# Optimization experiments

Hardware: AMD Instinct MI355X
Metric: run time of the kernel (lower is better)

The kernel has to match this reference:

```python
import jax, jax.numpy as jnp
import numpy as np

VOCAB, E, H, OUT = 32000, 128, 128, 16
N, L = 8192, 32


def setup_inputs() -> dict:
    key = jax.random.key(0)
    ks = jax.random.split(key, 12)
    s_lstm = 1.0 / np.sqrt(H)
    s_g1 = 1.0 / np.sqrt(2 * H)
    s_g2 = 1.0 / np.sqrt(OUT)
    return {
        "tokens": jax.random.randint(ks[0], (N, L), 0, VOCAB, dtype=jnp.int64)
        if jax.config.read("jax_enable_x64") else jax.random.randint(ks[0], (N, L), 0, VOCAB, dtype=jnp.int32),
        "adj": jax.random.uniform(ks[1], (N, N), dtype=jnp.float32) / N,
        "embed_W": jax.random.normal(ks[2], (VOCAB, E), dtype=jnp.float32),
        "W_ih": jax.random.uniform(ks[3], (4 * H, E), jnp.float32, -s_lstm, s_lstm),
        "W_hh": jax.random.uniform(ks[4], (4 * H, H), jnp.float32, -s_lstm, s_lstm),
        "b_ih": jax.random.uniform(ks[5], (4 * H,), jnp.float32, -s_lstm, s_lstm),
        "b_hh": jax.random.uniform(ks[6], (4 * H,), jnp.float32, -s_lstm, s_lstm),
        "gc1_W": jax.random.uniform(ks[7], (H, 2 * H), jnp.float32, -s_g1, s_g1),
        "gc1_b": jax.random.uniform(ks[8], (2 * H,), jnp.float32, -s_g1, s_g1),
        "gc2_W": jax.random.uniform(ks[9], (2 * H, OUT), jnp.float32, -s_g2, s_g2),
        "gc2_b": jax.random.uniform(ks[10], (OUT,), jnp.float32, -s_g2, s_g2),
    }


def _lstm_final_h(x, W_ih, W_hh, b_ih, b_hh):
    # x: [N, L, E] -> final hidden state [N, H] (torch gate order i,f,g,o)
    Hd = W_hh.shape[1]
    # precompute input projections for all timesteps: [L, N, 4H]
    xi = jnp.einsum('nle,ge->lng', x, W_ih) + b_ih + b_hh

    def step(carry, xt):
        h, c = carry
        gates = xt + h @ W_hh.T
        i, f, g, o = jnp.split(gates, 4, axis=-1)
        i, f, o = jax.nn.sigmoid(i), jax.nn.sigmoid(f), jax.nn.sigmoid(o)
        g = jnp.tanh(g)
        c = f * c + i * g
        h = o * jnp.tanh(c)
        return (h, c), None

    n = x.shape[0]
    h0 = jnp.zeros((n, Hd), x.dtype)
    (h, _), _ = jax.lax.scan(step, (h0, h0), xi)
    return h


def reference(tokens, adj, embed_W, W_ih, W_hh, b_ih, b_hh, gc1_W, gc1_b, gc2_W, gc2_b):
    x = embed_W[tokens]                                  # [N, L, E]
    feat = _lstm_final_h(x, W_ih, W_hh, b_ih, b_hh)      # [N, H]
    h1 = jax.nn.relu(adj @ (feat @ gc1_W) + gc1_b)       # [N, 2H]
    logits = adj @ (h1 @ gc2_W) + gc2_b                  # [N, OUT]
    return jax.nn.log_softmax(logits, axis=1)
```

## Files before the change

kernel.cpp:

```cpp
#include <hip/hip_runtime.h>

typedef __attribute__((ext_vector_type(8))) short bf16x8;
typedef __attribute__((ext_vector_type(4))) float f32x4;

__device__ __forceinline__ short f2bf(float f){
  union { float f; unsigned u; } v; v.f = f;
  unsigned r = v.u + 0x7fffu + ((v.u >> 16) & 1u);
  return (short)(r >> 16);
}
__device__ __forceinline__ bf16x8 pack8(float4 a, float4 b){
  bf16x8 v;
  v[0]=f2bf(a.x); v[1]=f2bf(a.y); v[2]=f2bf(a.z); v[3]=f2bf(a.w);
  v[4]=f2bf(b.x); v[5]=f2bf(b.y); v[6]=f2bf(b.z); v[7]=f2bf(b.w);
  return v;
}
__device__ __forceinline__ f32x4 mfma16(bf16x8 a, bf16x8 b, f32x4 c){
  return __builtin_amdgcn_mfma_f32_16x16x32_bf16(a, b, c, 0, 0, 0);
}
__device__ __forceinline__ float sigm(float x){
  return __builtin_amdgcn_rcpf(1.f + __expf(-x));
}
__device__ __forceinline__ float tanh_(float x){
  return 1.f - 2.f*__builtin_amdgcn_rcpf(1.f + __expf(2.f*x));
}

__global__ __launch_bounds__(512,2) void lstm_kernel(
    const int* __restrict__ tokens, const float* __restrict__ embed,
    const float* __restrict__ Wih, const float* __restrict__ Whh,
    const float* __restrict__ bih, const float* __restrict__ bhh,
    float* __restrict__ feat)
{
  __shared__ short hbuf[2*32*128];
  __shared__ short xbuf[2*32*128];
  __shared__ int   tokbuf[32*32];
  const int tid  = threadIdx.x;
  const int wave = tid >> 6, lane = tid & 63;
  const int l15  = lane & 15, lhi = lane >> 4;
  const int nbase = blockIdx.x * 32;
  const int ucol  = wave*16 + l15;

  bf16x8 wihf[4][4], whhf[4][4];
  #pragma unroll
  for(int g=0; g<4; ++g){
    const float* wi = Wih + (size_t)(g*128 + ucol)*128;
    const float* wh = Whh + (size_t)(g*128 + ucol)*128;
    #pragma unroll
    for(int kt=0; kt<4; ++kt){
      int e0 = kt*32 + lhi*8;
      float4 a0 = *(const float4*)(wi+e0), a1 = *(const float4*)(wi+e0+4);
      float4 b0 = *(const float4*)(wh+e0), b1 = *(const float4*)(wh+e0+4);
      wihf[g][kt] = pack8(a0,a1);
      whhf[g][kt] = pack8(b0,b1);
    }
  }
  float bs[4];
  #pragma unroll
  for(int g=0; g<4; ++g) bs[g] = bih[g*128+ucol] + bhh[g*128+ucol];

  for(int i=tid; i<1024; i+=512) tokbuf[i] = tokens[(size_t)nbase*32 + i];

  float c[2][4], hreg[2][4];
  #pragma unroll
  for(int m=0;m<2;++m) for(int r=0;r<4;++r){ c[m][r]=0.f; hreg[m][r]=0.f; }

  *(bf16x8*)((char*)hbuf + tid*16) = (bf16x8){0,0,0,0,0,0,0,0};
  __syncthreads();

  const int srow = tid >> 4, sseg = tid & 15;
  {
    int tok = tokbuf[srow*32 + 0];
    const float* e = embed + (size_t)tok*128 + sseg*8;
    float4 a = *(const float4*)e, b = *(const float4*)(e+4);
    int byte = (srow*256 + sseg*16) ^ ((srow&7)<<4);
    *(bf16x8*)((char*)xbuf + byte) = pack8(a,b);
  }
  __syncthreads();

  float4 sa, sb;
  #pragma unroll 1
  for(int l=0; l<32; ++l){
    if(l < 31){
      int tok = tokbuf[srow*32 + l + 1];
      const float* e = embed + (size_t)tok*128 + sseg*8;
      sa = *(const float4*)e; sb = *(const float4*)(e+4);
    }
    const char* hb = (const char*)hbuf + (l&1)*8192;
    const char* xb = (const char*)xbuf + (l&1)*8192;
    f32x4 acc[2][4];
    #pragma unroll
    for(int m=0;m<2;++m) for(int g=0;g<4;++g) acc[m][g]=(f32x4){0.f,0.f,0.f,0.f};
    #pragma unroll
    for(int kt=0; kt<4; ++kt){
      int cbyte = kt*64 + lhi*16;
      int swz = (l15&7)<<4;
      int a0 = (l15*256 + cbyte) ^ swz;
      int a1 = ((16+l15)*256 + cbyte) ^ swz;
      bf16x8 h0 = *(const bf16x8*)(hb + a0);
      bf16x8 h1 = *(const bf16x8*)(hb + a1);
      bf16x8 x0 = *(const bf16x8*)(xb + a0);
      bf16x8 x1 = *(const bf16x8*)(xb + a1);
      #pragma unroll
      for(int g=0; g<4; ++g){
        acc[0][g]=mfma16(h0, whhf[g][kt], acc[0][g]);
        acc[1][g]=mfma16(h1, whhf[g][kt], acc[1][g]);
        acc[0][g]=mfma16(x0, wihf[g][kt], acc[0][g]);
        acc[1][g]=mfma16(x1, wihf[g][kt], acc[1][g]);
      }
    }
    char* hn = (char*)hbuf + ((l+1)&1)*8192;
    #pragma unroll
    for(int m=0;m<2;++m){
      #pragma unroll
      for(int r=0;r<4;++r){
        float gi = acc[m][0][r] + bs[0];
        float gf = acc[m][1][r] + bs[1];
        float gg = acc[m][2][r] + bs[2];
        float go = acc[m][3][r] + bs[3];
        float i_ = sigm(gi), f_ = sigm(gf), o_ = sigm(go), g_ = tanh_(gg);
        float cc = f_*c[m][r] + i_*g_;
        c[m][r] = cc;
        float hh = o_*tanh_(cc);
        hreg[m][r] = hh;
        int row = m*16 + lhi*4 + r;
        int wb = (row*256 + ucol*2) ^ ((row&7)<<4);
        *(short*)(hn + wb) = f2bf(hh);
      }
    }
    if(l < 31){
      int byte = ((l+1)&1)*8192 + ((srow*256 + sseg*16) ^ ((srow&7)<<4));
      *(bf16x8*)((char*)xbuf + byte) = pack8(sa,sb);
    }
    __syncthreads();
  }
  #pragma unroll
  for(int m=0;m<2;++m) for(int r=0;r<4;++r){
    int row = nbase + m*16 + lhi*4 + r;
    feat[(size_t)row*128 + ucol] = hreg[m][r];
  }
}

__global__ __launch_bounds__(256) void gc1_kernel(
  const float* __restrict__ feat, const float* __restrict__ W1,
  short* __restrict__ Y1t)
{
  __shared__ float fs[128][36];
  int tid = threadIdx.x; int nb = blockIdx.x*32;
  #pragma unroll
  for(int i=0;i<4;++i){
    int idx = i*256 + tid;
    float4 v = ((const float4*)(feat + (size_t)nb*128))[idx];
    int n = idx>>5, k0 = (idx&31)*4;
    fs[k0][n]=v.x; fs[k0+1][n]=v.y; fs[k0+2][n]=v.z; fs[k0+3][n]=v.w;
  }
  __syncthreads();
  float acc[32];
  #pragma unroll
  for(int n=0;n<32;++n) acc[n]=0.f;
  int j = tid;
  for(int k=0;k<128;++k){
    float w = W1[k*256 + j];
    #pragma unroll
    for(int n4=0;n4<8;++n4){
      float4 f = *(const float4*)&fs[k][n4*4];
      acc[n4*4+0]+=f.x*w; acc[n4*4+1]+=f.y*w; acc[n4*4+2]+=f.z*w; acc[n4*4+3]+=f.w*w;
    }
  }
  unsigned* dst = (unsigned*)(Y1t + (size_t)j*8192 + nb);
  #pragma unroll
  for(int n=0;n<16;++n){
    unsigned lo = (unsigned short)f2bf(acc[2*n]);
    unsigned hi = (unsigned short)f2bf(acc[2*n+1]);
    dst[n] = lo | (hi<<16);
  }
}

__global__ __launch_bounds__(512,2) void gemm1_kernel(
  const float* __restrict__ adj, const short* __restrict__ Y1t,
  float* __restrict__ part)
{
  __shared__ short As[2*128*128];
  int tid=threadIdx.x, lane=tid&63, wid=tid>>6;
  int wr=wid>>2, wc=wid&3, l15=lane&15, lhi=lane>>4;
  int rb=(blockIdx.x>>2)*128;
  int ks=blockIdx.x&3;
  size_t kb0=(size_t)ks*2048;
  f32x4 acc[4][4];
  #pragma unroll
  for(int m=0;m<4;++m) for(int n=0;n<4;++n) acc[m][n]=(f32x4){0.f,0.f,0.f,0.f};

  const int srow = tid>>2, sseg = tid&3;
  const float* asrc = adj + (size_t)(rb+srow)*8192 + kb0 + sseg*32;
  float4 r[8];
  {
    const float4* p = (const float4*)asrc;
    #pragma unroll
    for(int i=0;i<8;++i) r[i]=p[i];
  }
  #pragma unroll 1
  for(int t=0; t<16; ++t){
    char* dst = (char*)As + (t&1)*32768;
    #pragma unroll
    for(int q=0;q<4;++q){
      int byte = (srow*256 + (sseg*32+q*8)*2) ^ ((srow&7)<<4);
      *(bf16x8*)(dst + byte) = pack8(r[2*q], r[2*q+1]);
    }
    __syncthreads();
    if(t<15){
      const float4* p = (const float4*)(asrc + (t+1)*128);
      #pragma unroll
      for(int i=0;i<8;++i) r[i]=p[i];
    }
    const char* cur = (const char*)As + (t&1)*32768;
    #pragma unroll
    for(int kk=0;kk<4;++kk){
      bf16x8 af[4];
      #pragma unroll
      for(int m=0;m<4;++m){
        int row = wr*64 + m*16 + l15;
        int byte = (row*256 + (kk*32+lhi*8)*2) ^ ((row&7)<<4);
        af[m] = *(const bf16x8*)(cur + byte);
      }
      const short* yb = Y1t + kb0 + t*128 + kk*32 + lhi*8;
      #pragma unroll
      for(int n=0;n<4;++n){
        bf16x8 bfr = *(const bf16x8*)(yb + (size_t)(wc*64 + n*16 + l15)*8192);
        #pragma unroll
        for(int m=0;m<4;++m) acc[m][n]=mfma16(af[m], bfr, acc[m][n]);
      }
    }
    __syncthreads();
  }
  float* pb = part + ((size_t)ks*8192 + rb)*256;
  #pragma unroll
  for(int m=0;m<4;++m) for(int n=0;n<4;++n){
    int row0=wr*64+m*16+lhi*4, col=wc*64+n*16+l15;
    #pragma unroll
    for(int q=0;q<4;++q) pb[(size_t)(row0+q)*256+col]=acc[m][n][q];
  }
}

__global__ __launch_bounds__(256) void reduce_kernel(
  const float* __restrict__ part, const float* __restrict__ b1,
  const float* __restrict__ W2, float* __restrict__ Y2)
{
  __shared__ float h1s[8][256];
  __shared__ float w2s[256*16];
  int tid=threadIdx.x, rb=blockIdx.x*8;
  for(int i=tid;i<1024;i+=256) ((float4*)w2s)[i]=((const float4*)W2)[i];
  int r=tid>>5, cb=(tid&31)*8;
  const float* p0 = part + (size_t)(rb+r)*256 + cb;
  float a[8];
  #pragma unroll
  for(int q=0;q<8;++q) a[q]=0.f;
  #pragma unroll
  for(int ks=0;ks<4;++ks){
    const float* p = p0 + (size_t)ks*2097152;
    float4 u=((const float4*)p)[0], v=((const float4*)p)[1];
    a[0]+=u.x; a[1]+=u.y; a[2]+=u.z; a[3]+=u.w;
    a[4]+=v.x; a[5]+=v.y; a[6]+=v.z; a[7]+=v.w;
  }
  #pragma unroll
  for(int q=0;q<8;++q){
    float v = a[q] + b1[cb+q];
    h1s[r][cb+q] = v>0.f ? v : 0.f;
  }
  __syncthreads();
  if(tid<128){
    int rr=tid>>4, j=tid&15;
    float s=0.f;
    for(int k4=0;k4<64;++k4){
      float4 h = *(const float4*)&h1s[rr][k4*4];
      s += h.x*w2s[(k4*4+0)*16+j] + h.y*w2s[(k4*4+1)*16+j]
         + h.z*w2s[(k4*4+2)*16+j] + h.w*w2s[(k4*4+3)*16+j];
    }
    Y2[(size_t)(rb+rr)*16+j]=s;
  }
}

__global__ __launch_bounds__(256) void gemm2_kernel(
  const float* __restrict__ adj, const float* __restrict__ Y2,
  const float* __restrict__ b2, float* __restrict__ out)
{
  __shared__ float red[16][16];
  int tid=threadIdx.x, lane=tid&63, w=tid>>6;
  int rb=blockIdx.x*16;
  int rowb=rb + w*4;
  float acc[4][16];
  #pragma unroll
  for(int rr=0;rr<4;++rr) for(int j=0;j<16;++j) acc[rr][j]=0.f;
  const float* a0 = adj + (size_t)rowb*8192;
  #pragma unroll 1
  for(int it=0; it<32; ++it){
    int kb = it*256 + lane*4;
    float4 av[4];
    #pragma unroll
    for(int rr=0;rr<4;++rr) av[rr] = *(const float4*)(a0 + (size_t)rr*8192 + kb);
    #pragma unroll
    for(int kk=0;kk<4;++kk){
      const float* yr = Y2 + (size_t)(kb+kk)*16;
      float4 y0=*(const float4*)yr,      y1=*(const float4*)(yr+4);
      float4 y2v=*(const float4*)(yr+8), y3=*(const float4*)(yr+12);
      #pragma unroll
      for(int rr=0;rr<4;++rr){
        float a = (kk==0)?av[rr].x:(kk==1)?av[rr].y:(kk==2)?av[rr].z:av[rr].w;
        acc[rr][0] +=a*y0.x;  acc[rr][1] +=a*y0.y;  acc[rr][2] +=a*y0.z;  acc[rr][3] +=a*y0.w;
        acc[rr][4] +=a*y1.x;  acc[rr][5] +=a*y1.y;  acc[rr][6] +=a*y1.z;  acc[rr][7] +=a*y1.w;
        acc[rr][8] +=a*y2v.x; acc[rr][9] +=a*y2v.y; acc[rr][10]+=a*y2v.z; acc[rr][11]+=a*y2v.w;
        acc[rr][12]+=a*y3.x;  acc[rr][13]+=a*y3.y;  acc[rr][14]+=a*y3.z;  acc[rr][15]+=a*y3.w;
      }
    }
  }
  #pragma unroll
  for(int mask=32; mask; mask>>=1){
    #pragma unroll
    for(int rr=0;rr<4;++rr)
      #pragma unroll
      for(int j=0;j<16;++j)
        acc[rr][j] += __shfl_xor(acc[rr][j], mask);
  }
  if(lane==0){
    #pragma unroll
    for(int rr=0;rr<4;++rr)
      #pragma unroll
      for(int j=0;j<16;++j) red[w*4+rr][j]=acc[rr][j];
  }
  __syncthreads();
  int r2=tid>>4, j=tid&15;
  float logit = red[r2][j] + b2[j];
  float m = logit;
  for(int msk=8;msk;msk>>=1) m = fmaxf(m, __shfl_xor(m, msk, 16));
  float e = __expf(logit - m);
  float den = e;
  for(int msk=8;msk;msk>>=1) den += __shfl_xor(den, msk, 16);
  out[(size_t)(rb+r2)*16 + j] = logit - m - __logf(den);
}

extern "C" void kernel_launch(void* const* d_in, const int* in_sizes, int n_in,
                              void* d_out, int out_size, void* d_ws, size_t ws_size,
                              hipStream_t stream) {
  const int*   tokens = (const int*)d_in[0];
  const float* adj    = (const float*)d_in[1];
  const float* embed  = (const float*)d_in[2];
  const float* Wih    = (const float*)d_in[3];
  const float* Whh    = (const float*)d_in[4];
  const float* bih    = (const float*)d_in[5];
  const float* bhh    = (const float*)d_in[6];
  const float* W1     = (const float*)d_in[7];
  const float* b1     = (const float*)d_in[8];
  const float* W2     = (const float*)d_in[9];
  const float* b2     = (const float*)d_in[10];
  float* out = (float*)d_out;

  char* ws = (char*)d_ws;
  float* feat = (float*)ws;
  short* Y1t  = (short*)(ws + (4u<<20));
  float* part = (float*)(ws + (8u<<20));
  float* Y2   = (float*)(ws + (40u<<20));

  lstm_kernel  <<<dim3(256),  dim3(512), 0, stream>>>(tokens, embed, Wih, Whh, bih, bhh, feat);
  gc1_kernel   <<<dim3(256),  dim3(256), 0, stream>>>(feat, W1, Y1t);
  gemm1_kernel <<<dim3(256),  dim3(512), 0, stream>>>(adj, Y1t, part);
  reduce_kernel<<<dim3(1024), dim3(256), 0, stream>>>(part, b1, W2, Y2);
  gemm2_kernel <<<dim3(512),  dim3(256), 0, stream>>>(adj, Y2, b2, out);
}
```

Measured before the change: 759.6 us.

## Retile gemm1 to 64-row blocks, transpose Y2 and prefetch adj in gemm2

gemm1 now uses 64-row tiles with 256 threads and 512 blocks, so the grid covers more CUs, and each wave computes a 32x128 output slab. reduce_kernel writes Y2 transposed so gemm2 can read contiguous float4 per output column. gemm2 also prefetches the next adj chunk into registers to overlap global loads with FMAs. The cost is that gemm1 reloads Y1t fragments twice as often per row, and gemm2 needs more registers for the prefetch buffer.

```diff
diff --git a/kernel.cpp b/kernel.cpp
--- a/kernel.cpp
+++ b/kernel.cpp
@@ -174,19 +174,19 @@
   }
 }
 
-__global__ __launch_bounds__(512,2) void gemm1_kernel(
+__global__ __launch_bounds__(256,2) void gemm1_kernel(
   const float* __restrict__ adj, const short* __restrict__ Y1t,
   float* __restrict__ part)
 {
-  __shared__ short As[2*128*128];
+  __shared__ short As[2*64*128];
   int tid=threadIdx.x, lane=tid&63, wid=tid>>6;
-  int wr=wid>>2, wc=wid&3, l15=lane&15, lhi=lane>>4;
-  int rb=(blockIdx.x>>2)*128;
+  int wr=wid>>1, wc=wid&1, l15=lane&15, lhi=lane>>4;
+  int rb=(blockIdx.x>>2)*64;
   int ks=blockIdx.x&3;
   size_t kb0=(size_t)ks*2048;
-  f32x4 acc[4][4];
-  #pragma unroll
-  for(int m=0;m<4;++m) for(int n=0;n<4;++n) acc[m][n]=(f32x4){0.f,0.f,0.f,0.f};
+  f32x4 acc[2][8];
+  #pragma unroll
+  for(int m=0;m<2;++m) for(int n=0;n<8;++n) acc[m][n]=(f32x4){0.f,0.f,0.f,0.f};
 
   const int srow = tid>>2, sseg = tid&3;
   const float* asrc = adj + (size_t)(rb+srow)*8192 + kb0 + sseg*32;
@@ -198,7 +198,7 @@
   }
   #pragma unroll 1
   for(int t=0; t<16; ++t){
-    char* dst = (char*)As + (t&1)*32768;
+    char* dst = (char*)As + (t&1)*16384;
     #pragma unroll
     for(int q=0;q<4;++q){
       int byte = (srow*256 + (sseg*32+q*8)*2) ^ ((srow&7)<<4);
@@ -210,30 +210,30 @@
       #pragma unroll
       for(int i=0;i<8;++i) r[i]=p[i];
     }
-    const char* cur = (const char*)As + (t&1)*32768;
+    const char* cur = (const char*)As + (t&1)*16384;
     #pragma unroll
     for(int kk=0;kk<4;++kk){
-      bf16x8 af[4];
-      #pragma unroll
-      for(int m=0;m<4;++m){
-        int row = wr*64 + m*16 + l15;
+      bf16x8 af[2];
+      #pragma unroll
+      for(int m=0;m<2;++m){
+        int row = wr*32 + m*16 + l15;
         int byte = (row*256 + (kk*32+lhi*8)*2) ^ ((row&7)<<4);
         af[m] = *(const bf16x8*)(cur + byte);
       }
       const short* yb = Y1t + kb0 + t*128 + kk*32 + lhi*8;
       #pragma unroll
-      for(int n=0;n<4;++n){
-        bf16x8 bfr = *(const bf16x8*)(yb + (size_t)(wc*64 + n*16 + l15)*8192);
+      for(int n=0;n<8;++n){
+        bf16x8 bfr = *(const bf16x8*)(yb + (size_t)(wc*128 + n*16 + l15)*8192);
         #pragma unroll
-        for(int m=0;m<4;++m) acc[m][n]=mfma16(af[m], bfr, acc[m][n]);
+        for(int m=0;m<2;++m) acc[m][n]=mfma16(af[m], bfr, acc[m][n]);
       }
     }
     __syncthreads();
   }
   float* pb = part + ((size_t)ks*8192 + rb)*256;
   #pragma unroll
-  for(int m=0;m<4;++m) for(int n=0;n<4;++n){
-    int row0=wr*64+m*16+lhi*4, col=wc*64+n*16+l15;
+  for(int m=0;m<2;++m) for(int n=0;n<8;++n){
+    int row0=wr*32+m*16+lhi*4, col=wc*128+n*16+l15;
     #pragma unroll
     for(int q=0;q<4;++q) pb[(size_t)(row0+q)*256+col]=acc[m][n][q];
   }
@@ -241,7 +241,7 @@
 
 __global__ __launch_bounds__(256) void reduce_kernel(
   const float* __restrict__ part, const float* __restrict__ b1,
-  const float* __restrict__ W2, float* __restrict__ Y2)
+  const float* __restrict__ W2, float* __restrict__ Y2t)
 {
   __shared__ float h1s[8][256];
   __shared__ float w2s[256*16];
@@ -273,12 +273,12 @@
       s += h.x*w2s[(k4*4+0)*16+j] + h.y*w2s[(k4*4+1)*16+j]
          + h.z*w2s[(k4*4+2)*16+j] + h.w*w2s[(k4*4+3)*16+j];
     }
-    Y2[(size_t)(rb+rr)*16+j]=s;
-  }
-}
-
-__global__ __launch_bounds__(256) void gemm2_kernel(
-  const float* __restrict__ adj, const float* __restrict__ Y2,
+    Y2t[(size_t)j*8192 + rb + rr] = s;
+  }
+}
+
+__global__ __launch_bounds__(256,2) void gemm2_kernel(
+  const float* __restrict__ adj, const float* __restrict__ Y2t,
   const float* __restrict__ b2, float* __restrict__ out)
 {
   __shared__ float red[16][16];
@@ -289,26 +289,27 @@
   #pragma unroll
   for(int rr=0;rr<4;++rr) for(int j=0;j<16;++j) acc[rr][j]=0.f;
   const float* a0 = adj + (size_t)rowb*8192;
+  float4 av[4];
+  #pragma unroll
+  for(int rr=0;rr<4;++rr) av[rr] = *(const float4*)(a0 + (size_t)rr*8192 + lane*4);
   #pragma unroll 1
   for(int it=0; it<32; ++it){
+    float4 nv[4];
+    if(it<31){
+      int kbn = (it+1)*256 + lane*4;
+      #pragma unroll
+      for(int rr=0;rr<4;++rr) nv[rr] = *(const float4*)(a0 + (size_t)rr*8192 + kbn);
+    }
     int kb = it*256 + lane*4;
-    float4 av[4];
-    #pragma unroll
-    for(int rr=0;rr<4;++rr) av[rr] = *(const float4*)(a0 + (size_t)rr*8192 + kb);
-    #pragma unroll
-    for(int kk=0;kk<4;++kk){
-      const float* yr = Y2 + (size_t)(kb+kk)*16;
-      float4 y0=*(const float4*)yr,      y1=*(const float4*)(yr+4);
-      float4 y2v=*(const float4*)(yr+8), y3=*(const float4*)(yr+12);
-      #pragma unroll
-      for(int rr=0;rr<4;++rr){
-        float a = (kk==0)?av[rr].x:(kk==1)?av[rr].y:(kk==2)?av[rr].z:av[rr].w;
-        acc[rr][0] +=a*y0.x;  acc[rr][1] +=a*y0.y;  acc[rr][2] +=a*y0.z;  acc[rr][3] +=a*y0.w;
-        acc[rr][4] +=a*y1.x;  acc[rr][5] +=a*y1.y;  acc[rr][6] +=a*y1.z;  acc[rr][7] +=a*y1.w;
-        acc[rr][8] +=a*y2v.x; acc[rr][9] +=a*y2v.y; acc[rr][10]+=a*y2v.z; acc[rr][11]+=a*y2v.w;
-        acc[rr][12]+=a*y3.x;  acc[rr][13]+=a*y3.y;  acc[rr][14]+=a*y3.z;  acc[rr][15]+=a*y3.w;
-      }
-    }
+    #pragma unroll
+    for(int j=0;j<16;++j){
+      float4 y = *(const float4*)(Y2t + (size_t)j*8192 + kb);
+      #pragma unroll
+      for(int rr=0;rr<4;++rr)
+        acc[rr][j] += av[rr].x*y.x + av[rr].y*y.y + av[rr].z*y.z + av[rr].w*y.w;
+    }
+    #pragma unroll
+    for(int rr=0;rr<4;++rr) av[rr]=nv[rr];
   }
   #pragma unroll
   for(int mask=32; mask; mask>>=1){
@@ -355,11 +356,11 @@
   float* feat = (float*)ws;
   short* Y1t  = (short*)(ws + (4u<<20));
   float* part = (float*)(ws + (8u<<20));
-  float* Y2   = (float*)(ws + (40u<<20));
+  float* Y2t  = (float*)(ws + (40u<<20));
 
   lstm_kernel  <<<dim3(256),  dim3(512), 0, stream>>>(tokens, embed, Wih, Whh, bih, bhh, feat);
   gc1_kernel   <<<dim3(256),  dim3(256), 0, stream>>>(feat, W1, Y1t);
-  gemm1_kernel <<<dim3(256),  dim3(512), 0, stream>>>(adj, Y1t, part);
-  reduce_kernel<<<dim3(1024), dim3(256), 0, stream>>>(part, b1, W2, Y2);
-  gemm2_kernel <<<dim3(512),  dim3(256), 0, stream>>>(adj, Y2, b2, out);
-}
+  gemm1_kernel <<<dim3(512),  dim3(256), 0, stream>>>(adj, Y1t, part);
+  reduce_kernel<<<dim3(1024), dim3(256), 0, stream>>>(part, b1, W2, Y2t);
+  gemm2_kernel <<<dim3(512),  dim3(256), 0, stream>>>(adj, Y2t, b2, out);
+}
```

Result: faster. 695.1 us (-8.5%).
